# Performance work log

Hardware: AMD Instinct MI355X
Metric: run time of the kernel (lower is better)

## Reference

```python
import jax, jax.numpy as jnp
import numpy as np

NEG_SLOPE = 0.2


def gat_conv(x, src, dst, W, asrc, adst, b):
    """Single-head PyG-style GATConv with self-loops.
    x: [N, din], src/dst: [E] int, W: [din, d], asrc/adst: [d], b: [d]."""
    N = x.shape[0]
    h = x @ W  # [N, d]
    alpha_s = h @ asrc  # [N]
    alpha_d = h @ adst  # [N]
    # add self loops so every node has at least one incoming edge
    loop = jnp.arange(N, dtype=src.dtype)
    srcf = jnp.concatenate([src, loop])
    dstf = jnp.concatenate([dst, loop])
    e = jax.nn.leaky_relu(alpha_s[srcf] + alpha_d[dstf], NEG_SLOPE)  # [E+N]
    m = jax.ops.segment_max(e, dstf, num_segments=N)
    ex = jnp.exp(e - m[dstf])
    denom = jax.ops.segment_sum(ex, dstf, num_segments=N)
    alpha = ex / denom[dstf]
    out = jax.ops.segment_sum(h[srcf] * alpha[:, None], dstf, num_segments=N)
    return out + b


def sdgnn_forward(x, edges, Wg, a_src, a_dst, bg, W1, b1, W2, b2):
    L = Wg.shape[0]
    R = Wg.shape[1]
    for l in range(L):
        feats = [x]
        for r in range(R):
            feats.append(gat_conv(x, edges[r, 0], edges[r, 1],
                                  Wg[l, r], a_src[l, r], a_dst[l, r], bg[l, r]))
        combined = jnp.concatenate(feats, axis=1)  # [N, 5*d]
        x = jnp.tanh(combined @ W1[l] + b1[l]) @ W2[l] + b2[l]
    return x


def setup_inputs() -> dict:
    key = jax.random.key(0)
    ks = jax.random.split(key, 8)
    N, D, E, L, R = 100000, 64, 1000000, 2, 4
    scale = 0.15  # ~kaiming for d=64
    x = jax.random.normal(ks[0], (N, D), dtype=jnp.float32)
    edges = jax.random.randint(ks[1], (R, 2, E), 0, N, dtype=jnp.int64)
    Wg = jax.random.normal(ks[2], (L, R, D, D), dtype=jnp.float32) * scale
    a_src = jax.random.normal(ks[3], (L, R, D), dtype=jnp.float32) * scale
    a_dst = jax.random.normal(ks[4], (L, R, D), dtype=jnp.float32) * scale
    bg = jnp.zeros((L, R, D), dtype=jnp.float32)
    W1 = jax.random.normal(ks[5], (L, 5 * D, D), dtype=jnp.float32) * 0.08
    b1 = jnp.zeros((L, D), dtype=jnp.float32)
    W2 = jax.random.normal(ks[6], (L, D, D), dtype=jnp.float32) * scale
    b2 = jnp.zeros((L, D), dtype=jnp.float32)
    return {"x": x, "edges": edges, "Wg": Wg, "a_src": a_src, "a_dst": a_dst,
            "bg": bg, "W1": W1, "b1": b1, "W2": W2, "b2": b2}


def reference(x, edges, Wg, a_src, a_dst, bg, W1, b1, W2, b2):
    return sdgnn_forward(x, edges, Wg, a_src, a_dst, bg, W1, b1, W2, b2)
```

## Files before the change

### kernel.cpp

```cpp
#include <hip/hip_runtime.h>
#include <hip/hip_bf16.h>
#include <math.h>

#define DD 64
#define RREL 4
#define LLAY 2
#define NEG_SLOPE 0.2f
#define EPB 4096
#define BSH 10
#define BSZ 1024

typedef __attribute__((ext_vector_type(8))) short short8;
typedef __attribute__((ext_vector_type(4))) short short4v;
typedef __attribute__((ext_vector_type(4))) float float4v;

__device__ __forceinline__ float lrelu(float x) { return x > 0.f ? x : NEG_SLOPE * x; }

__device__ __forceinline__ unsigned short f2bf(float f) {
    unsigned int u = __float_as_uint(f);
    return (unsigned short)((u + 0x7FFFu + ((u >> 16) & 1u)) >> 16);
}
__device__ __forceinline__ float bf2f(unsigned short u) {
    return __uint_as_float((unsigned int)u << 16);
}
__device__ __forceinline__ float bflo(unsigned int u) { return __uint_as_float(u << 16); }
__device__ __forceinline__ float bfhi(unsigned int u) {
    return __uint_as_float(u & 0xffff0000u);
}

__global__ void k_wvec(const float* __restrict__ Wg, const float* __restrict__ asrc,
                       const float* __restrict__ adst, float* __restrict__ wsrc,
                       float* __restrict__ wdst) {
    int idx = blockIdx.x * blockDim.x + threadIdx.x;
    if (idx >= LLAY * RREL * DD) return;
    int k = idx & 63;
    int lr = idx >> 6;
    const float* W = Wg + (size_t)lr * DD * DD;
    const float* as = asrc + lr * DD;
    const float* ad = adst + lr * DD;
    float s1 = 0.f, s2 = 0.f;
#pragma unroll
    for (int j = 0; j < DD; j++) {
        float w = W[k * DD + j];
        s1 += w * as[j];
        s2 += w * ad[j];
    }
    wsrc[idx] = s1;
    wdst[idx] = s2;
}

__global__ void k_prep(const float* __restrict__ Wg, const float* __restrict__ W1,
                       const float* __restrict__ W2, unsigned short* __restrict__ WgT,
                       unsigned short* __restrict__ W1T, unsigned short* __restrict__ W2T) {
    int idx = blockIdx.x * blockDim.x + threadIdx.x;
    if (idx < 8 * 4096) {
        int lr = idx >> 12, rem = idx & 4095, n = rem >> 6, k = rem & 63;
        WgT[idx] = f2bf(Wg[(size_t)lr * 4096 + k * 64 + n]);
    } else if (idx < 32768 + 2 * 64 * 320) {
        int i = idx - 32768;
        int l = i / 20480, rem = i % 20480, n = rem / 320, kk = rem % 320;
        int src;
        if (kk < 64) src = kk;
        else {
            int r = (kk - 64) >> 6, f = (kk - 64) & 63;
            src = 64 + r * 64 + ((f & 3) * 16) + (f >> 2);
        }
        W1T[i] = f2bf(W1[(size_t)l * 20480 + src * 64 + n]);
    } else if (idx < 32768 + 40960 + 2 * 4096) {
        int i = idx - 73728;
        int l = i >> 12, rem = i & 4095, n = rem >> 6, k = rem & 63;
        W2T[i] = f2bf(W2[(size_t)l * 4096 + k * 64 + n]);
    }
}

__global__ void k_copy_x(const float* __restrict__ x, unsigned short* __restrict__ combined,
                         int N) {
    int i = blockIdx.x * blockDim.x + threadIdx.x;
    if (i >= N * 32) return;
    int row = i >> 5, c2 = i & 31;
    float2 v = *(const float2*)(x + (size_t)row * DD + c2 * 2);
    unsigned int p = (unsigned int)f2bf(v.x) | ((unsigned int)f2bf(v.y) << 16);
    *(unsigned int*)(combined + (size_t)row * 320 + c2 * 2) = p;
}

__global__ void k_zero(int* __restrict__ p, int n) {
    int i = blockIdx.x * blockDim.x + threadIdx.x;
    if (i < n) p[i] = 0;
}

__global__ __launch_bounds__(256) void k_bhist(const int* __restrict__ edges,
                                               int* __restrict__ btot, int E, int NB) {
    int r = blockIdx.y;
    int e0 = blockIdx.x * EPB;
    int t = threadIdx.x;
    __shared__ int lh[128];
    for (int i = t; i < 128; i += 256) lh[i] = 0;
    __syncthreads();
    const int* dstp = edges + (size_t)r * 2 * E + E;
#pragma unroll
    for (int i = 0; i < EPB / 256; i++) {
        int e = e0 + t + 256 * i;
        if (e < E) atomicAdd(&lh[dstp[e] >> BSH], 1);
    }
    __syncthreads();
    for (int i = t; i < NB; i += 256) {
        int c = lh[i];
        if (c) atomicAdd(&btot[r * NB + i], c);
    }
}

__global__ void k_bscan(const int* __restrict__ btot, int* __restrict__ bucketoff,
                        int* __restrict__ bpos, int* __restrict__ csr_ptr, int N, int E, int NB) {
    int r = threadIdx.x;
    if (r >= RREL) return;
    int run = 0;
    for (int b = 0; b < NB; b++) {
        bucketoff[r * (NB + 1) + b] = run;
        bpos[r * NB + b] = run;
        run += btot[r * NB + b];
    }
    bucketoff[r * (NB + 1) + NB] = run;
    csr_ptr[(size_t)r * (N + 1) + N] = E;
}

__global__ __launch_bounds__(256) void k_binscatter(const int* __restrict__ edges,
                                                    int* __restrict__ bpos,
                                                    unsigned int* __restrict__ packed, int E,
                                                    int NB) {
    int r = blockIdx.y;
    int e0 = blockIdx.x * EPB;
    int t = threadIdx.x;
    __shared__ int lh[128], lbase[128];
    for (int i = t; i < 128; i += 256) lh[i] = 0;
    __syncthreads();
    const int* srcp = edges + (size_t)r * 2 * E;
    const int* dstp = srcp + E;
    int md[EPB / 256], ms[EPB / 256];
#pragma unroll
    for (int i = 0; i < EPB / 256; i++) {
        int e = e0 + t + 256 * i;
        int d = -1, s = 0;
        if (e < E) {
            d = dstp[e];
            s = srcp[e];
            atomicAdd(&lh[d >> BSH], 1);
        }
        md[i] = d;
        ms[i] = s;
    }
    __syncthreads();
    for (int i = t; i < NB; i += 256) {
        int c = lh[i];
        lbase[i] = c ? atomicAdd(&bpos[r * NB + i], c) : 0;
        lh[i] = 0;
    }
    __syncthreads();
#pragma unroll
    for (int i = 0; i < EPB / 256; i++) {
        if (md[i] >= 0) {
            int b = md[i] >> BSH;
            int p = lbase[b] + atomicAdd(&lh[b], 1);
            packed[(size_t)r * E + p] =
                ((unsigned int)(md[i] & (BSZ - 1)) << 17) | (unsigned int)ms[i];
        }
    }
}

__global__ __launch_bounds__(256) void k_bucket_sort(const unsigned int* __restrict__ packed,
                                                     const int* __restrict__ bucketoff,
                                                     int* __restrict__ csr_ptr,
                                                     int* __restrict__ csr_src, int N, int E,
                                                     int NB) {
    int r = blockIdx.y, b = blockIdx.x;
    int t = threadIdx.x;
    __shared__ int pos[BSZ];
    __shared__ int tsum[256];
    int base = bucketoff[r * (NB + 1) + b];
    int cnt = bucketoff[r * (NB + 1) + b + 1] - base;
    const unsigned int* pk = packed + (size_t)r * E + base;
    for (int i = t; i < BSZ; i += 256) pos[i] = 0;
    __syncthreads();
    for (int i = t; i < cnt; i += 256) atomicAdd(&pos[pk[i] >> 17], 1);
    __syncthreads();
    int v[4];
    int s = 0;
#pragma unroll
    for (int i = 0; i < 4; i++) {
        v[i] = pos[t * 4 + i];
        s += v[i];
    }
    tsum[t] = s;
    __syncthreads();
    for (int off = 1; off < 256; off <<= 1) {
        int add = (t >= off) ? tsum[t - off] : 0;
        __syncthreads();
        tsum[t] += add;
        __syncthreads();
    }
    int run = tsum[t] - s;
    __syncthreads();
#pragma unroll
    for (int i = 0; i < 4; i++) {
        int node_l = t * 4 + i;
        pos[node_l] = run;
        int node = b * BSZ + node_l;
        if (node < N) csr_ptr[(size_t)r * (N + 1) + node] = base + run;
        run += v[i];
    }
    __syncthreads();
    for (int i = t; i < cnt; i += 256) {
        unsigned int p = pk[i];
        int d = p >> 17;
        int sidx = p & 0x1FFFF;
        int loc = atomicAdd(&pos[d], 1);
        csr_src[(size_t)r * E + base + loc] = sidx;
    }
}


__global__ __launch_bounds__(256, 3) void k_hgemm(const unsigned short* __restrict__ X,
                                                  const unsigned short* __restrict__ WgTl,
                                                  const float* __restrict__ wsrcl,
                                                  const float* __restrict__ wdstl,
                                                  unsigned short* __restrict__ h4,
                                                  float* __restrict__ as4,
                                                  float* __restrict__ ad4, int N) {
    __shared__ __align__(16) unsigned short Xb[256][72];
    __shared__ __align__(16) unsigned short Wb[64][72];
    __shared__ float wsS[4][64], wdS[4][64];
    int tid = threadIdx.x, wave = tid >> 6, lane = tid & 63;
    int l15 = lane & 15, q = lane >> 4;
    int row0 = blockIdx.x * 256;
#pragma unroll
    for (int i = 0; i < 8; i++) {
        int f = tid + 256 * i;
        int rr = f >> 3, seg = f & 7;
        int grow = row0 + rr;
        short8 v = (short8){0, 0, 0, 0, 0, 0, 0, 0};
        if (grow < N) v = *(const short8*)(X + (size_t)grow * 320 + seg * 8);
        *(short8*)&Xb[rr][seg * 8] = v;
    }
    wsS[tid >> 6][tid & 63] = wsrcl[tid];
    wdS[tid >> 6][tid & 63] = wdstl[tid];
    __syncthreads();
    short8 afr[4][2];
#pragma unroll
    for (int mt = 0; mt < 4; mt++)
#pragma unroll
        for (int ks = 0; ks < 2; ks++)
            afr[mt][ks] = *(const short8*)&Xb[wave * 64 + mt * 16 + l15][ks * 32 + q * 8];
    {
        int grow = row0 + tid;
        float s[4] = {0.f, 0.f, 0.f, 0.f}, d[4] = {0.f, 0.f, 0.f, 0.f};
#pragma unroll
        for (int seg = 0; seg < 8; seg++) {
            short8 v = *(const short8*)&Xb[tid][seg * 8];
#pragma unroll
            for (int j = 0; j < 8; j++) {
                float xv = bf2f((unsigned short)v[j]);
                int k = seg * 8 + j;
#pragma unroll
                for (int r = 0; r < 4; r++) {
                    s[r] += xv * wsS[r][k];
                    d[r] += xv * wdS[r][k];
                }
            }
        }
        if (grow < N) {
#pragma unroll
            for (int r = 0; r < 4; r++) {
                as4[(size_t)r * N + grow] = s[r];
                ad4[(size_t)r * N + grow] = d[r];
            }
        }
    }
    for (int r = 0; r < 4; r++) {
        __syncthreads();
#pragma unroll
        for (int i = 0; i < 2; i++) {
            int f = tid + 256 * i;
            int n = f >> 3, seg = f & 7;
            *(short8*)&Wb[n][seg * 8] = *(const short8*)(WgTl + r * 4096 + n * 64 + seg * 8);
        }
        __syncthreads();
        short8 bfr[4][2];
#pragma unroll
        for (int nt = 0; nt < 4; nt++)
#pragma unroll
            for (int ks = 0; ks < 2; ks++)
                bfr[nt][ks] = *(const short8*)&Wb[nt * 16 + l15][ks * 32 + q * 8];
        float4v acc[4][4];
#pragma unroll
        for (int mt = 0; mt < 4; mt++)
#pragma unroll
            for (int nt = 0; nt < 4; nt++) acc[mt][nt] = (float4v){0.f, 0.f, 0.f, 0.f};
#pragma unroll
        for (int mt = 0; mt < 4; mt++)
#pragma unroll
            for (int nt = 0; nt < 4; nt++) {
                acc[mt][nt] = __builtin_amdgcn_mfma_f32_16x16x32_bf16(afr[mt][0], bfr[nt][0],
                                                                     acc[mt][nt], 0, 0, 0);
                acc[mt][nt] = __builtin_amdgcn_mfma_f32_16x16x32_bf16(afr[mt][1], bfr[nt][1],
                                                                     acc[mt][nt], 0, 0, 0);
            }
        unsigned short* hr = h4 + (size_t)r * N * 64;
#pragma unroll
        for (int mt = 0; mt < 4; mt++) {
            int rowb = row0 + wave * 64 + mt * 16 + q * 4;
#pragma unroll
            for (int reg = 0; reg < 4; reg++) {
                int row = rowb + reg;
                if (row < N) {
                    short4v sv;
                    sv[0] = (short)f2bf(acc[mt][0][reg]);
                    sv[1] = (short)f2bf(acc[mt][1][reg]);
                    sv[2] = (short)f2bf(acc[mt][2][reg]);
                    sv[3] = (short)f2bf(acc[mt][3][reg]);
                    *(short4v*)&hr[(size_t)row * 64 + l15 * 4] = sv;
                }
            }
        }
    }
}

template <bool BFOUT>
__global__ __launch_bounds__(256, 3) void k_mlp(const unsigned short* __restrict__ X,
                                                const unsigned short* __restrict__ W1Tl,
                                                const float* __restrict__ b1,
                                                const unsigned short* __restrict__ W2Tl,
                                                const float* __restrict__ b2,
                                                unsigned short* __restrict__ Ybf,
                                                float* __restrict__ Yf, int ldy, int N) {
    __shared__ __align__(16) unsigned short Xb[256][72];
    __shared__ __align__(16) unsigned short Wb[64][72];
    int tid = threadIdx.x, wave = tid >> 6, lane = tid & 63;
    int l15 = lane & 15, q = lane >> 4;
    int row0 = blockIdx.x * 256;
    float4v acc[4][4];
#pragma unroll
    for (int mt = 0; mt < 4; mt++)
#pragma unroll
        for (int nt = 0; nt < 4; nt++) acc[mt][nt] = (float4v){0.f, 0.f, 0.f, 0.f};
    for (int kc = 0; kc < 320; kc += 64) {
        __syncthreads();
#pragma unroll
        for (int i = 0; i < 8; i++) {
            int f = tid + 256 * i;
            int rr = f >> 3, seg = f & 7;
            int grow = row0 + rr;
            short8 v = (short8){0, 0, 0, 0, 0, 0, 0, 0};
            if (grow < N) v = *(const short8*)(X + (size_t)grow * 320 + kc + seg * 8);
            *(short8*)&Xb[rr][seg * 8] = v;
        }
#pragma unroll
        for (int i = 0; i < 2; i++) {
            int f = tid + 256 * i;
            int n = f >> 3, seg = f & 7;
            *(short8*)&Wb[n][seg * 8] = *(const short8*)(W1Tl + n * 320 + kc + seg * 8);
        }
        __syncthreads();
        short8 bfr[4][2];
#pragma unroll
        for (int nt = 0; nt < 4; nt++)
#pragma unroll
            for (int ks = 0; ks < 2; ks++)
                bfr[nt][ks] = *(const short8*)&Wb[nt * 16 + l15][ks * 32 + q * 8];
#pragma unroll
        for (int mt = 0; mt < 4; mt++) {
            short8 a0 = *(const short8*)&Xb[wave * 64 + mt * 16 + l15][q * 8];
            short8 a1 = *(const short8*)&Xb[wave * 64 + mt * 16 + l15][32 + q * 8];
#pragma unroll
            for (int nt = 0; nt < 4; nt++) {
                acc[mt][nt] =
                    __builtin_amdgcn_mfma_f32_16x16x32_bf16(a0, bfr[nt][0], acc[mt][nt], 0, 0, 0);
                acc[mt][nt] =
                    __builtin_amdgcn_mfma_f32_16x16x32_bf16(a1, bfr[nt][1], acc[mt][nt], 0, 0, 0);
            }
        }
    }
    __syncthreads();
#pragma unroll
    for (int mt = 0; mt < 4; mt++) {
        int rlb = wave * 64 + mt * 16 + q * 4;
#pragma unroll
        for (int reg = 0; reg < 4; reg++) {
#pragma unroll
            for (int nt = 0; nt < 4; nt++) {
                int n = nt * 16 + l15;
                Xb[rlb + reg][n] = f2bf(tanhf(acc[mt][nt][reg] + b1[n]));
            }
        }
    }
#pragma unroll
    for (int i = 0; i < 2; i++) {
        int f = tid + 256 * i;
        int n = f >> 3, seg = f & 7;
        *(short8*)&Wb[n][seg * 8] = *(const short8*)(W2Tl + n * 64 + seg * 8);
    }
    __syncthreads();
    short8 bfr[4][2];
#pragma unroll
    for (int nt = 0; nt < 4; nt++)
#pragma unroll
        for (int ks = 0; ks < 2; ks++)
            bfr[nt][ks] = *(const short8*)&Wb[nt * 16 + l15][ks * 32 + q * 8];
    float4v acc2[4][4];
#pragma unroll
    for (int mt = 0; mt < 4; mt++)
#pragma unroll
        for (int nt = 0; nt < 4; nt++) acc2[mt][nt] = (float4v){0.f, 0.f, 0.f, 0.f};
#pragma unroll
    for (int mt = 0; mt < 4; mt++) {
        short8 a0 = *(const short8*)&Xb[wave * 64 + mt * 16 + l15][q * 8];
        short8 a1 = *(const short8*)&Xb[wave * 64 + mt * 16 + l15][32 + q * 8];
#pragma unroll
        for (int nt = 0; nt < 4; nt++) {
            acc2[mt][nt] =
                __builtin_amdgcn_mfma_f32_16x16x32_bf16(a0, bfr[nt][0], acc2[mt][nt], 0, 0, 0);
            acc2[mt][nt] =
                __builtin_amdgcn_mfma_f32_16x16x32_bf16(a1, bfr[nt][1], acc2[mt][nt], 0, 0, 0);
        }
    }
#pragma unroll
    for (int mt = 0; mt < 4; mt++) {
        int rowb = row0 + wave * 64 + mt * 16 + q * 4;
#pragma unroll
        for (int reg = 0; reg < 4; reg++) {
            int row = rowb + reg;
            if (row < N) {
#pragma unroll
                for (int nt = 0; nt < 4; nt++) {
                    int n = nt * 16 + l15;
                    float v = acc2[mt][nt][reg] + b2[n];
                    if (BFOUT)
                        Ybf[(size_t)row * ldy + n] = f2bf(v);
                    else
                        Yf[(size_t)row * ldy + n] = v;
                }
            }
        }
    }
}

__device__ void gat_node_fullwave(int node, const int* __restrict__ csr_ptr,
                                  const int* __restrict__ csr_src,
                                  const unsigned short* __restrict__ h,
                                  const float* __restrict__ as_,
                                  const float* __restrict__ ad_, float bgv,
                                  unsigned short* __restrict__ out, int ldo, int lane) {
    float adv = ad_[node];
    float e_self = lrelu(as_[node] + adv);
    int beg = csr_ptr[node], end = csr_ptr[node + 1];
    int cnt = end - beg;

    if (cnt <= 64) {
        int s = 0;
        float e_lane = -3.0e38f;
        if (lane < cnt) {
            s = csr_src[beg + lane];
            e_lane = lrelu(as_[s] + adv);
        }
        float m = fmaxf(e_lane, e_self);
#pragma unroll
        for (int off = 32; off; off >>= 1) m = fmaxf(m, __shfl_xor(m, off));
        float p = (lane < cnt) ? expf(e_lane - m) : 0.f;
        float ssum = p;
#pragma unroll
        for (int off = 32; off; off >>= 1) ssum += __shfl_xor(ssum, off);
        float p_self = expf(e_self - m);
        float inv = 1.f / (ssum + p_self);
        float alpha = p * inv;
        float acc = p_self * inv * bf2f(h[(size_t)node * DD + lane]);
        for (int j0 = 0; j0 < cnt; ++j0) {
            int ss = __shfl(s, j0);
            float aa = __shfl(alpha, j0);
            acc += aa * bf2f(h[(size_t)ss * DD + lane]);
        }
        out[(size_t)node * ldo + lane] = f2bf(acc + bgv);
        return;
    }

    float m = e_self;
    for (int j = beg + lane; j < end; j += 64) m = fmaxf(m, lrelu(as_[csr_src[j]] + adv));
#pragma unroll
    for (int off = 32; off; off >>= 1) m = fmaxf(m, __shfl_xor(m, off));
    float ssum = 0.f;
    for (int j = beg + lane; j < end; j += 64) ssum += expf(lrelu(as_[csr_src[j]] + adv) - m);
#pragma unroll
    for (int off = 32; off; off >>= 1) ssum += __shfl_xor(ssum, off);
    ssum += expf(e_self - m);
    float inv = 1.f / ssum;
    float acc = expf(e_self - m) * inv * bf2f(h[(size_t)node * DD + lane]);
    for (int j0 = beg; j0 < end; j0 += 64) {
        int j = j0 + lane;
        int s = 0;
        float alpha = 0.f;
        if (j < end) {
            s = csr_src[j];
            alpha = expf(lrelu(as_[s] + adv) - m) * inv;
        }
        int c = end - j0;
        if (c > 64) c = 64;
        for (int t = 0; t < c; ++t) {
            int ss = __shfl(s, t);
            float aa = __shfl(alpha, t);
            acc += aa * bf2f(h[(size_t)ss * DD + lane]);
        }
    }
    out[(size_t)node * ldo + lane] = f2bf(acc + bgv);
}

__global__ __launch_bounds__(256) void k_gat(const int* __restrict__ csr_ptr4,
                                             const int* __restrict__ csr_src4,
                                             const unsigned short* __restrict__ h4,
                                             const float* __restrict__ as4,
                                             const float* __restrict__ ad4,
                                             const float* __restrict__ bg4,
                                             unsigned short* __restrict__ outbase, int ldo,
                                             int N, int E) {
    __shared__ int lsa_s[4][4][32];
    __shared__ float lsa_p[4][4][32];
    int lb = blockIdx.x;
    int r = (lb & 7) >> 1;
    int idx = ((lb >> 3) << 1) + (lb & 1);
    int wave = threadIdx.x >> 6, lane = threadIdx.x & 63;
    int qd = lane >> 4, lq = lane & 15;
    int nodeA = idx * 16 + wave * 4;
    if (nodeA >= N) return;
    int node = nodeA + qd;
    bool act = node < N;

    const int* csr_ptr = csr_ptr4 + (size_t)r * (N + 1);
    const int* csr_src = csr_src4 + (size_t)r * E;
    const unsigned short* h = h4 + (size_t)r * N * 64;
    const float* as_ = as4 + (size_t)r * N;
    const float* ad_ = ad4 + (size_t)r * N;
    const float* bg = bg4 + (size_t)r * DD;
    unsigned short* out = outbase + (size_t)64 * r;

    int beg = 0, cnt = 0;
    if (act) {
        beg = csr_ptr[node];
        cnt = csr_ptr[node + 1] - beg;
    }
    int m2 = max(cnt, __shfl_xor(cnt, 16));
    int vmax = __builtin_amdgcn_readfirstlane(max(m2, __shfl_xor(m2, 32)));

    if (vmax <= 32) {
        bool in0 = lq < cnt;
        int s0 = 0;
        if (in0) s0 = csr_src[beg + lq];
        lsa_s[wave][qd][lq] = s0;
        bool need2 = vmax > 16;
        bool in1 = false;
        int s1 = 0;
        if (need2) {
            in1 = (lq + 16) < cnt;
            if (in1) s1 = csr_src[beg + lq + 16];
            lsa_s[wave][qd][lq + 16] = s1;
        }
        float adv = act ? ad_[node] : 0.f;
        float e_self = act ? lrelu(as_[node] + adv) : 0.f;
        float asl0 = in0 ? as_[s0] : 0.f;
        float p0 = in0 ? __expf(lrelu(asl0 + adv)) : 0.f;
        lsa_p[wave][qd][lq] = p0;
        float p1 = 0.f;
        if (need2) {
            float asl1 = in1 ? as_[s1] : 0.f;
            p1 = in1 ? __expf(lrelu(asl1 + adv)) : 0.f;
            lsa_p[wave][qd][lq + 16] = p1;
        }
        float p_self = __expf(e_self);

        const char* hb = (const char*)h;
        unsigned lane8 = (unsigned)(lq << 3);
        uint2 hvs = make_uint2(0u, 0u);
        if (act) hvs = *(const uint2*)(hb + (((unsigned)node) << 7) + lane8);

        float a0 = 0.f, a1 = 0.f, a2 = 0.f, a3 = 0.f;
        float c0 = 0.f, c1 = 0.f, c2 = 0.f, c3 = 0.f;
        const int* sp = &lsa_s[wave][qd][0];
        const float* pp = &lsa_p[wave][qd][0];
        for (int j0 = 0; j0 < vmax; j0 += 8) {
#pragma unroll
            for (int g = 0; g < 2; g++) {
                if (j0 + g * 4 < vmax) {
#pragma unroll
                    for (int u = 0; u < 4; u++) {
                        int sv = sp[j0 + g * 4 + u];
                        unsigned voff = ((unsigned)sv << 7) + lane8;
                        uint2 hv = *(const uint2*)(hb + voff);
                        float pw = pp[j0 + g * 4 + u];
                        if (u & 1) {
                            c0 += pw * bflo(hv.x);
                            c1 += pw * bfhi(hv.x);
                            c2 += pw * bflo(hv.y);
                            c3 += pw * bfhi(hv.y);
                        } else {
                            a0 += pw * bflo(hv.x);
                            a1 += pw * bfhi(hv.x);
                            a2 += pw * bflo(hv.y);
                            a3 += pw * bfhi(hv.y);
                        }
                    }
                }
            }
        }
        float ssum = p0 + p1;
#pragma unroll
        for (int off = 8; off; off >>= 1) ssum += __shfl_xor(ssum, off);
        float inv = __builtin_amdgcn_rcpf(ssum + p_self);

        if (act) {
            float o0 = (a0 + c0 + p_self * bflo(hvs.x)) * inv + bg[lq];
            float o1 = (a1 + c1 + p_self * bfhi(hvs.x)) * inv + bg[16 + lq];
            float o2 = (a2 + c2 + p_self * bflo(hvs.y)) * inv + bg[32 + lq];
            float o3 = (a3 + c3 + p_self * bfhi(hvs.y)) * inv + bg[48 + lq];
            uint2 pck;
            pck.x = (unsigned int)f2bf(o0) | ((unsigned int)f2bf(o1) << 16);
            pck.y = (unsigned int)f2bf(o2) | ((unsigned int)f2bf(o3) << 16);
            *(uint2*)(out + (size_t)node * ldo + 4 * lq) = pck;
        }
        return;
    }

    float bgv = bg[((lane & 3) << 4) | (lane >> 2)];
#pragma unroll
    for (int k = 0; k < 4; k++) {
        if (nodeA + k < N)
            gat_node_fullwave(nodeA + k, csr_ptr, csr_src, h, as_, ad_, bgv, out, ldo, lane);
    }
}

extern "C" void kernel_launch(void* const* d_in, const int* in_sizes, int n_in,
                              void* d_out, int out_size, void* d_ws, size_t ws_size,
                              hipStream_t stream) {
    const float* x = (const float*)d_in[0];
    const int* edges = (const int*)d_in[1];
    const float* Wg = (const float*)d_in[2];
    const float* a_src = (const float*)d_in[3];
    const float* a_dst = (const float*)d_in[4];
    const float* bg = (const float*)d_in[5];
    const float* W1 = (const float*)d_in[6];
    const float* b1 = (const float*)d_in[7];
    const float* W2 = (const float*)d_in[8];
    const float* b2 = (const float*)d_in[9];
    float* out = (float*)d_out;

    const int N = in_sizes[0] / DD;
    const int E = in_sizes[1] / (2 * RREL);
    const int NB = (N + BSZ - 1) >> BSH;

    size_t off = 0;
    auto alloc = [&](size_t bytes) {
        size_t o = off;
        off = (off + bytes + 255) & ~(size_t)255;
        return o;
    };
    char* ws = (char*)d_ws;
    unsigned short* combined = (unsigned short*)(ws + alloc((size_t)N * 320 * 2));
    unsigned short* h4 = (unsigned short*)(ws + alloc((size_t)4 * N * 64 * 2));
    float* wsrc = (float*)(ws + alloc(LLAY * RREL * DD * 4));
    float* wdst = (float*)(ws + alloc(LLAY * RREL * DD * 4));
    unsigned short* WgT = (unsigned short*)(ws + alloc(8 * 4096 * 2));
    unsigned short* W1T = (unsigned short*)(ws + alloc(2 * 64 * 320 * 2));
    unsigned short* W2T = (unsigned short*)(ws + alloc(2 * 4096 * 2));
    int* btot = (int*)(ws + alloc((size_t)RREL * NB * 4));
    int* bucketoff = (int*)(ws + alloc((size_t)RREL * (NB + 1) * 4));
    int* bpos = (int*)(ws + alloc((size_t)RREL * NB * 4));
    unsigned int* packed = (unsigned int*)(ws + alloc((size_t)RREL * E * 4));
    int* csr_ptr = (int*)(ws + alloc((size_t)RREL * (N + 1) * 4));
    int* csr_src = (int*)(ws + alloc((size_t)RREL * E * 4));
    (void)ws_size;
    float* as4 = (float*)packed;
    float* ad4 = as4 + (size_t)4 * N;

    const int ebblocks = (E + EPB - 1) / EPB;

    k_zero<<<dim3((RREL * NB + 255) / 256), dim3(256), 0, stream>>>(btot, RREL * NB);
    k_wvec<<<dim3(2), dim3(256), 0, stream>>>(Wg, a_src, a_dst, wsrc, wdst);
    k_prep<<<dim3(320), dim3(256), 0, stream>>>(Wg, W1, W2, WgT, W1T, W2T);
    k_copy_x<<<dim3((N * 32 + 255) / 256), dim3(256), 0, stream>>>(x, combined, N);
    k_bhist<<<dim3(ebblocks, RREL), dim3(256), 0, stream>>>(edges, btot, E, NB);
    k_bscan<<<dim3(1), dim3(64), 0, stream>>>(btot, bucketoff, bpos, csr_ptr, N, E, NB);
    k_binscatter<<<dim3(ebblocks, RREL), dim3(256), 0, stream>>>(edges, bpos, packed, E, NB);
    k_bucket_sort<<<dim3(NB, RREL), dim3(256), 0, stream>>>(packed, bucketoff, csr_ptr, csr_src,
                                                            N, E, NB);

    const int gemm_blocks = (N + 255) / 256;
    const int bpr = (N + 15) / 16;
    const int gat_grid = 8 * ((bpr + 1) / 2);

    for (int l = 0; l < LLAY; l++) {
        k_hgemm<<<dim3(gemm_blocks), dim3(256), 0, stream>>>(
            combined, WgT + (size_t)l * 4 * 4096, wsrc + l * 256, wdst + l * 256, h4, as4, ad4, N);
        k_gat<<<dim3(gat_grid), dim3(256), 0, stream>>>(
            csr_ptr, csr_src, h4, as4, ad4, bg + (size_t)l * RREL * DD,
            combined + 64, 320, N, E);
        if (l == LLAY - 1) {
            k_mlp<false><<<dim3(gemm_blocks), dim3(256), 0, stream>>>(
                combined, W1T + (size_t)l * 20480, b1 + l * DD, W2T + (size_t)l * 4096,
                b2 + l * DD, nullptr, out, DD, N);
        } else {
            k_mlp<true><<<dim3(gemm_blocks), dim3(256), 0, stream>>>(
                combined, W1T + (size_t)l * 20480, b1 + l * DD, W2T + (size_t)l * 4096,
                b2 + l * DD, combined, nullptr, 320, N);
        }
    }
}
```

Baseline: 466.4 us.

## Process eight nodes per wave with 16-byte row loads in GAT kernel

Remaps the GAT aggregation so each wave handles eight destination nodes, with eight lanes per node, instead of four nodes with sixteen lanes each. Each lane now gathers 16 bytes (eight bf16 features) per neighbour row instead of 8 bytes, and the shared-memory neighbour and weight tables are transposed so lanes of different nodes read adjacent entries. The aim is fewer, wider gather loads and twice as many nodes in flight per wave, at the cost of more serial neighbour iterations per lane, a single accumulator chain, and a larger wave-wide max degree deciding when the fast path applies.

Result: faster. 454.6 us (-2.5%).

```diff
diff --git a/kernel.cpp b/kernel.cpp
--- a/kernel.cpp
+++ b/kernel.cpp
@@ -518,16 +518,16 @@
                                              const float* __restrict__ bg4,
                                              unsigned short* __restrict__ outbase, int ldo,
                                              int N, int E) {
-    __shared__ int lsa_s[4][4][32];
-    __shared__ float lsa_p[4][4][32];
+    __shared__ int lsa_s[4][32][8];
+    __shared__ float lsa_p[4][32][8];
     int lb = blockIdx.x;
     int r = (lb & 7) >> 1;
     int idx = ((lb >> 3) << 1) + (lb & 1);
     int wave = threadIdx.x >> 6, lane = threadIdx.x & 63;
-    int qd = lane >> 4, lq = lane & 15;
-    int nodeA = idx * 16 + wave * 4;
+    int oct = lane >> 3, lq = lane & 7;
+    int nodeA = idx * 32 + wave * 8;
     if (nodeA >= N) return;
-    int node = nodeA + qd;
+    int node = nodeA + oct;
     bool act = node < N;
 
     const int* csr_ptr = csr_ptr4 + (size_t)r * (N + 1);
@@ -543,90 +543,110 @@
         beg = csr_ptr[node];
         cnt = csr_ptr[node + 1] - beg;
     }
-    int m2 = max(cnt, __shfl_xor(cnt, 16));
+    int m2 = max(cnt, __shfl_xor(cnt, 8));
+    m2 = max(m2, __shfl_xor(m2, 16));
     int vmax = __builtin_amdgcn_readfirstlane(max(m2, __shfl_xor(m2, 32)));
 
     if (vmax <= 32) {
-        bool in0 = lq < cnt;
-        int s0 = 0;
-        if (in0) s0 = csr_src[beg + lq];
-        lsa_s[wave][qd][lq] = s0;
-        bool need2 = vmax > 16;
-        bool in1 = false;
-        int s1 = 0;
-        if (need2) {
-            in1 = (lq + 16) < cnt;
-            if (in1) s1 = csr_src[beg + lq + 16];
-            lsa_s[wave][qd][lq + 16] = s1;
+        bool in0 = lq < cnt, in1 = false, in2 = false, in3 = false;
+        int s0 = in0 ? csr_src[beg + lq] : 0, s1 = 0, s2 = 0, s3 = 0;
+        lsa_s[wave][lq][oct] = s0;
+        if (vmax > 8) {
+            in1 = (lq + 8) < cnt;
+            s1 = in1 ? csr_src[beg + lq + 8] : 0;
+            lsa_s[wave][lq + 8][oct] = s1;
+        }
+        if (vmax > 16) {
+            in2 = (lq + 16) < cnt;
+            s2 = in2 ? csr_src[beg + lq + 16] : 0;
+            lsa_s[wave][lq + 16][oct] = s2;
+        }
+        if (vmax > 24) {
+            in3 = (lq + 24) < cnt;
+            s3 = in3 ? csr_src[beg + lq + 24] : 0;
+            lsa_s[wave][lq + 24][oct] = s3;
         }
         float adv = act ? ad_[node] : 0.f;
         float e_self = act ? lrelu(as_[node] + adv) : 0.f;
-        float asl0 = in0 ? as_[s0] : 0.f;
-        float p0 = in0 ? __expf(lrelu(asl0 + adv)) : 0.f;
-        lsa_p[wave][qd][lq] = p0;
-        float p1 = 0.f;
-        if (need2) {
-            float asl1 = in1 ? as_[s1] : 0.f;
-            p1 = in1 ? __expf(lrelu(asl1 + adv)) : 0.f;
-            lsa_p[wave][qd][lq + 16] = p1;
+        float p0 = in0 ? __expf(lrelu(as_[s0] + adv)) : 0.f;
+        lsa_p[wave][lq][oct] = p0;
+        float psum = p0;
+        if (vmax > 8) {
+            float p = in1 ? __expf(lrelu(as_[s1] + adv)) : 0.f;
+            lsa_p[wave][lq + 8][oct] = p;
+            psum += p;
+        }
+        if (vmax > 16) {
+            float p = in2 ? __expf(lrelu(as_[s2] + adv)) : 0.f;
+            lsa_p[wave][lq + 16][oct] = p;
+            psum += p;
+        }
+        if (vmax > 24) {
+            float p = in3 ? __expf(lrelu(as_[s3] + adv)) : 0.f;
+            lsa_p[wave][lq + 24][oct] = p;
+            psum += p;
         }
         float p_self = __expf(e_self);
 
         const char* hb = (const char*)h;
-        unsigned lane8 = (unsigned)(lq << 3);
-        uint2 hvs = make_uint2(0u, 0u);
-        if (act) hvs = *(const uint2*)(hb + (((unsigned)node) << 7) + lane8);
+        unsigned lane16 = (unsigned)(lq << 4);
+        uint4 hvs = make_uint4(0u, 0u, 0u, 0u);
+        if (act) hvs = *(const uint4*)(hb + (((unsigned)node) << 7) + lane16);
 
         float a0 = 0.f, a1 = 0.f, a2 = 0.f, a3 = 0.f;
-        float c0 = 0.f, c1 = 0.f, c2 = 0.f, c3 = 0.f;
-        const int* sp = &lsa_s[wave][qd][0];
-        const float* pp = &lsa_p[wave][qd][0];
+        float a4 = 0.f, a5 = 0.f, a6 = 0.f, a7 = 0.f;
+        const int(*sp)[8] = &lsa_s[wave][0];
+        const float(*pp)[8] = &lsa_p[wave][0];
         for (int j0 = 0; j0 < vmax; j0 += 8) {
 #pragma unroll
             for (int g = 0; g < 2; g++) {
                 if (j0 + g * 4 < vmax) {
 #pragma unroll
                     for (int u = 0; u < 4; u++) {
-                        int sv = sp[j0 + g * 4 + u];
-                        unsigned voff = ((unsigned)sv << 7) + lane8;
-                        uint2 hv = *(const uint2*)(hb + voff);
-                        float pw = pp[j0 + g * 4 + u];
-                        if (u & 1) {
-                            c0 += pw * bflo(hv.x);
-                            c1 += pw * bfhi(hv.x);
-                            c2 += pw * bflo(hv.y);
-                            c3 += pw * bfhi(hv.y);
-                        } else {
-                            a0 += pw * bflo(hv.x);
-                            a1 += pw * bfhi(hv.x);
-                            a2 += pw * bflo(hv.y);
-                            a3 += pw * bfhi(hv.y);
-                        }
+                        int sv = sp[j0 + g * 4 + u][oct];
+                        unsigned voff = ((unsigned)sv << 7) + lane16;
+                        uint4 hv = *(const uint4*)(hb + voff);
+                        float pw = pp[j0 + g * 4 + u][oct];
+                        a0 += pw * bflo(hv.x);
+                        a1 += pw * bfhi(hv.x);
+                        a2 += pw * bflo(hv.y);
+                        a3 += pw * bfhi(hv.y);
+                        a4 += pw * bflo(hv.z);
+                        a5 += pw * bfhi(hv.z);
+                        a6 += pw * bflo(hv.w);
+                        a7 += pw * bfhi(hv.w);
                     }
                 }
             }
         }
-        float ssum = p0 + p1;
-#pragma unroll
-        for (int off = 8; off; off >>= 1) ssum += __shfl_xor(ssum, off);
+        float ssum = psum;
+#pragma unroll
+        for (int off = 4; off; off >>= 1) ssum += __shfl_xor(ssum, off);
         float inv = __builtin_amdgcn_rcpf(ssum + p_self);
 
         if (act) {
-            float o0 = (a0 + c0 + p_self * bflo(hvs.x)) * inv + bg[lq];
-            float o1 = (a1 + c1 + p_self * bfhi(hvs.x)) * inv + bg[16 + lq];
-            float o2 = (a2 + c2 + p_self * bflo(hvs.y)) * inv + bg[32 + lq];
-            float o3 = (a3 + c3 + p_self * bfhi(hvs.y)) * inv + bg[48 + lq];
-            uint2 pck;
+            int b0 = 2 * lq;
+            float o0 = (a0 + p_self * bflo(hvs.x)) * inv + bg[b0];
+            float o1 = (a1 + p_self * bfhi(hvs.x)) * inv + bg[16 + b0];
+            float o2 = (a2 + p_self * bflo(hvs.y)) * inv + bg[32 + b0];
+            float o3 = (a3 + p_self * bfhi(hvs.y)) * inv + bg[48 + b0];
+            float o4 = (a4 + p_self * bflo(hvs.z)) * inv + bg[b0 + 1];
+            float o5 = (a5 + p_self * bfhi(hvs.z)) * inv + bg[16 + b0 + 1];
+            float o6 = (a6 + p_self * bflo(hvs.w)) * inv + bg[32 + b0 + 1];
+            float o7 = (a7 + p_self * bfhi(hvs.w)) * inv + bg[48 + b0 + 1];
+            uint4 pck;
             pck.x = (unsigned int)f2bf(o0) | ((unsigned int)f2bf(o1) << 16);
             pck.y = (unsigned int)f2bf(o2) | ((unsigned int)f2bf(o3) << 16);
-            *(uint2*)(out + (size_t)node * ldo + 4 * lq) = pck;
+            pck.z = (unsigned int)f2bf(o4) | ((unsigned int)f2bf(o5) << 16);
+            pck.w = (unsigned int)f2bf(o6) | ((unsigned int)f2bf(o7) << 16);
+            *(uint4*)(out + (size_t)node * ldo + 8 * lq) = pck;
         }
         return;
     }
 
     float bgv = bg[((lane & 3) << 4) | (lane >> 2)];
 #pragma unroll
-    for (int k = 0; k < 4; k++) {
+    for (int k = 0; k < 8; k++) {
         if (nodeA + k < N)
             gat_node_fullwave(nodeA + k, csr_ptr, csr_src, h, as_, ad_, bgv, out, ldo, lane);
     }
@@ -688,7 +708,7 @@
                                                             N, E, NB);
 
     const int gemm_blocks = (N + 255) / 256;
-    const int bpr = (N + 15) / 16;
+    const int bpr = (N + 31) / 32;
     const int gat_grid = 8 * ((bpr + 1) / 2);
 
     for (int l = 0; l < LLAY; l++) {
```
